# Optimization experiments

Measured on AMD Instinct MI355X. Metric: run time of the kernel, lower is better.

The kernel has to match this reference:

```python
import jax, jax.numpy as jnp
import numpy as np

D_MODEL = 1024
D_STATE = 16
D_CONV = 4
EXPAND = 2
D_INNER = EXPAND * D_MODEL        # 2048
DT_RANK = D_MODEL // 16           # ceil(1024/16) = 64
B, L = 2, 2048


def setup_inputs() -> dict:
    key = jax.random.key(0)
    ks = jax.random.split(key, 8)
    def init(k, shape, fan_in):
        return jax.random.normal(k, shape, jnp.float32) / np.sqrt(fan_in).astype(np.float32)
    x = jax.random.normal(ks[0], (B, L, D_MODEL), jnp.float32)
    W_in = init(ks[1], (2 * D_INNER, D_MODEL), D_MODEL)
    conv_w = init(ks[2], (D_INNER, 1, D_CONV), D_CONV)      # depthwise kernel (O, I/groups, K)
    conv_b = jnp.zeros((D_INNER,), jnp.float32)
    W_x = init(ks[3], (DT_RANK + 2 * D_STATE, D_INNER), D_INNER)
    W_dt = init(ks[4], (D_INNER, DT_RANK), DT_RANK)
    b_dt = jnp.zeros((D_INNER,), jnp.float32)
    A_log = jnp.log(jnp.tile(jnp.arange(1, D_STATE + 1, dtype=jnp.float32), (D_INNER, 1)))
    D_param = jnp.ones((D_INNER,), jnp.float32)
    W_out = init(ks[5], (D_MODEL, D_INNER), D_INNER)
    return {"x": x, "W_in": W_in, "conv_w": conv_w, "conv_b": conv_b,
            "W_x": W_x, "W_dt": W_dt, "b_dt": b_dt, "A_log": A_log,
            "D_param": D_param, "W_out": W_out}


def _mamba_forward(x, W_in, conv_w, conv_b, W_x, W_dt, b_dt, A_log, D_param, W_out):
    b, l, d = x.shape
    # in_proj -> split into ssm path and gate residual
    x_and_res = x @ W_in.T                               # [b, l, 2*d_inner]
    x_m, res = jnp.split(x_and_res, 2, axis=-1)
    # causal depthwise conv1d (torch pads both sides d_conv-1 then slices [:l] == left-pad causal conv)
    xc = jnp.transpose(x_m, (0, 2, 1))                   # [b, d_inner, l]
    xc = jax.lax.conv_general_dilated(
        xc, conv_w, window_strides=(1,), padding=[(D_CONV - 1, 0)],
        dimension_numbers=('NCH', 'OIH', 'NCH'), feature_group_count=D_INNER)
    xc = xc + conv_b[None, :, None]
    x_m = jax.nn.silu(jnp.transpose(xc, (0, 2, 1)))      # [b, l, d_inner]
    # ssm parameterization
    A = -jnp.exp(A_log)                                  # [d_inner, n]
    x_dbl = x_m @ W_x.T                                  # [b, l, dt_rank + 2n]
    dlt, Bm, Cm = jnp.split(x_dbl, [DT_RANK, DT_RANK + D_STATE], axis=-1)
    delta = jax.nn.softplus(dlt @ W_dt.T + b_dt)         # [b, l, d_inner]
    # selective scan over time
    def step(h, inp):
        d_i, B_i, C_i, x_i = inp                         # [b,d_in], [b,n], [b,n], [b,d_in]
        dA = jnp.exp(d_i[..., None] * A)                 # [b, d_in, n]
        h = dA * h + (d_i * x_i)[..., None] * B_i[:, None, :]
        y = jnp.einsum('bdn,bn->bd', h, C_i)
        return h, y
    h0 = jnp.zeros((b, D_INNER, D_STATE), x.dtype)
    seq = (jnp.transpose(delta, (1, 0, 2)), jnp.transpose(Bm, (1, 0, 2)),
           jnp.transpose(Cm, (1, 0, 2)), jnp.transpose(x_m, (1, 0, 2)))
    _, ys = jax.lax.scan(step, h0, seq)                  # [l, b, d_inner]
    y = jnp.transpose(ys, (1, 0, 2)) + D_param * x_m     # [b, l, d_inner]
    y = y * jax.nn.silu(res)
    return y @ W_out.T                                   # [b, l, d_model]


def reference(x, W_in, conv_w, conv_b, W_x, W_dt, b_dt, A_log, D_param, W_out):
    return _mamba_forward(x, W_in, conv_w, conv_b, W_x, W_dt, b_dt, A_log, D_param, W_out)
```

## Files before the change

kernel.cpp:

```cpp
#include <hip/hip_runtime.h>

typedef unsigned short u16;
typedef __attribute__((ext_vector_type(8))) short bf16x8;
typedef __attribute__((ext_vector_type(4))) float f32x4;

#define B_SZ   2
#define L_SZ   2048
#define DM     1024
#define DI     2048
#define NST    16
#define RNK    64
#define TOK    (B_SZ * L_SZ)
#define NC     128
#define CLEN   (L_SZ / NC)
#define XDS    128
#define KSPL   8

__device__ __forceinline__ float bf2f(u16 u) {
    return __uint_as_float(((unsigned int)u) << 16);
}
__device__ __forceinline__ u16 f2bf(float f) {
    unsigned int x = __float_as_uint(f);
    x += 0x7fffu + ((x >> 16) & 1u);
    return (u16)(x >> 16);
}
__device__ __forceinline__ float silu(float v) {
    return v / (1.f + __expf(-v));
}
__device__ __forceinline__ float softplus_f(float v) {
    return (v > 20.f) ? v : log1pf(__expf(v));
}
__device__ __forceinline__ void gload16(const u16* g, u16* l) {
    __builtin_amdgcn_global_load_lds(
        (const __attribute__((address_space(1))) void*)g,
        (__attribute__((address_space(3))) void*)l, 16, 0, 0);
}
__device__ __forceinline__ ushort4 cvt4(const float4 v) {
    ushort4 o;
    o.x = f2bf(v.x); o.y = f2bf(v.y); o.z = f2bf(v.z); o.w = f2bf(v.w);
    return o;
}

#define Q_XB   1048576
#define Q_WIN  (Q_XB + 1048576)
#define Q_WOUT (Q_WIN + 524288)
#define Q_WX   (Q_WOUT + 65536)
#define Q_WDT  (Q_WX + 32768)
__global__ __launch_bounds__(256)
void cvt_all(const float4* __restrict__ x,  const float4* __restrict__ Wi,
             const float4* __restrict__ Wo, const float4* __restrict__ Wx,
             const float4* __restrict__ Wd,
             ushort4* __restrict__ xb,  ushort4* __restrict__ Wib,
             ushort4* __restrict__ Wob, ushort4* __restrict__ Wxb,
             ushort4* __restrict__ Wdb)
{
    const int i = blockIdx.x * 256 + threadIdx.x;
    if (i < Q_XB) {
        xb[i] = cvt4(x[i]);
    } else if (i < Q_WIN) {
        const int j = i - Q_XB;  Wib[j] = cvt4(Wi[j]);
    } else if (i < Q_WOUT) {
        const int j = i - Q_WIN; Wob[j] = cvt4(Wo[j]);
    } else if (i < Q_WX) {
        const int j = i - Q_WOUT;
        const int row = (j * 4) >> 11;
        if (row < 96) Wxb[j] = cvt4(Wx[j]);
        else          Wxb[j] = (ushort4){0, 0, 0, 0};
    } else if (i < Q_WDT) {
        const int j = i - Q_WX;  Wdb[j] = cvt4(Wd[j]);
    }
}

template<int EPI>
__global__ __launch_bounds__(256, 2)
void gemm_bt(const u16* __restrict__ A, const u16* __restrict__ B,
             const int K, const int N,
             u16* __restrict__ out0, u16* __restrict__ out1,
             float* __restrict__ outF, const float* __restrict__ bias)
{
    __shared__ u16 sA[128 * 32];
    __shared__ u16 sB[128 * 32];

    const int tid  = threadIdx.x;
    const int rowBase = blockIdx.x << 7;
    const int colBase = blockIdx.y << 7;
    const int wave = tid >> 6, lane = tid & 63;
    const int wm = (wave >> 1) << 6;
    const int wn = (wave & 1) << 6;
    const int lrow = lane & 15, quad = lane >> 4;

    const int sr  = tid >> 2;
    const int skc = tid & 3;
    const u16* Ap = A + (size_t)(rowBase + sr) * K + skc * 8;
    const u16* Bp = B + (size_t)(colBase + sr) * K + skc * 8;
    const size_t rowJump = (size_t)64 * K;
    u16* lA0 = &sA[tid * 8];
    u16* lA1 = &sA[64 * 32 + tid * 8];
    u16* lB0 = &sB[tid * 8];
    u16* lB1 = &sB[64 * 32 + tid * 8];

    f32x4 acc[4][4];
#pragma unroll
    for (int i = 0; i < 4; ++i)
#pragma unroll
        for (int j = 0; j < 4; ++j) acc[i][j] = (f32x4){0.f, 0.f, 0.f, 0.f};

    const int KT = K >> 5;
    for (int kt = 0; kt < KT; ++kt) {
        const int ko = kt * 32;
        gload16(Ap + ko, lA0);
        gload16(Ap + ko + rowJump, lA1);
        gload16(Bp + ko, lB0);
        gload16(Bp + ko + rowJump, lB1);
        __syncthreads();

        bf16x8 af[4], bfr[4];
#pragma unroll
        for (int i = 0; i < 4; ++i)
            af[i] = *(const bf16x8*)&sA[(wm + i * 16 + lrow) * 32 + quad * 8];
#pragma unroll
        for (int j = 0; j < 4; ++j)
            bfr[j] = *(const bf16x8*)&sB[(wn + j * 16 + lrow) * 32 + quad * 8];

#pragma unroll
        for (int i = 0; i < 4; ++i)
#pragma unroll
            for (int j = 0; j < 4; ++j)
                acc[i][j] = __builtin_amdgcn_mfma_f32_16x16x32_bf16(
                    bfr[j], af[i], acc[i][j], 0, 0, 0);
        __syncthreads();
    }

#pragma unroll
    for (int i = 0; i < 4; ++i) {
        const int token = rowBase + wm + i * 16 + lrow;
#pragma unroll
        for (int j = 0; j < 4; ++j) {
            const int ch = colBase + wn + j * 16 + quad * 4;
            const f32x4 v = acc[i][j];
            if (EPI == 0) {
                *(float4*)&outF[(size_t)token * N + ch] =
                    (float4){v[0], v[1], v[2], v[3]};
            } else if (EPI == 2) {
                const float4 bb = *(const float4*)&bias[ch];
                ushort4 o;
                o.x = f2bf(softplus_f(v[0] + bb.x));
                o.y = f2bf(softplus_f(v[1] + bb.y));
                o.z = f2bf(softplus_f(v[2] + bb.z));
                o.w = f2bf(softplus_f(v[3] + bb.w));
                *(ushort4*)&out0[(size_t)token * N + ch] = o;
            } else {
                if (ch < DI) {
                    ushort4 o;
                    o.x = f2bf(v[0]); o.y = f2bf(v[1]);
                    o.z = f2bf(v[2]); o.w = f2bf(v[3]);
                    *(ushort4*)&out0[(size_t)token * DI + ch] = o;
                } else {
                    ushort4 o;
                    o.x = f2bf(silu(v[0])); o.y = f2bf(silu(v[1]));
                    o.z = f2bf(silu(v[2])); o.w = f2bf(silu(v[3]));
                    *(ushort4*)&out1[(size_t)token * DI + (ch - DI)] = o;
                }
            }
        }
    }
}

__global__ __launch_bounds__(256, 2)
void gemm_xdbl(const u16* __restrict__ A, const u16* __restrict__ B,
               float* __restrict__ part)
{
    __shared__ u16 sA[128 * 32];
    __shared__ u16 sB[128 * 32];

    const int tid  = threadIdx.x;
    const int rowBase = blockIdx.x << 7;
    const int ks   = blockIdx.y;
    const int k0   = ks * (DI / KSPL);
    const int wave = tid >> 6, lane = tid & 63;
    const int wm = (wave >> 1) << 6;
    const int wn = (wave & 1) << 6;
    const int lrow = lane & 15, quad = lane >> 4;

    const int sr  = tid >> 2;
    const int skc = tid & 3;
    const u16* Ap = A + (size_t)(rowBase + sr) * DI + k0 + skc * 8;
    const u16* Bp = B + (size_t)sr * DI + k0 + skc * 8;
    const size_t rowJump = (size_t)64 * DI;
    u16* lA0 = &sA[tid * 8];
    u16* lA1 = &sA[64 * 32 + tid * 8];
    u16* lB0 = &sB[tid * 8];
    u16* lB1 = &sB[64 * 32 + tid * 8];

    f32x4 acc[4][4];
#pragma unroll
    for (int i = 0; i < 4; ++i)
#pragma unroll
        for (int j = 0; j < 4; ++j) acc[i][j] = (f32x4){0.f, 0.f, 0.f, 0.f};

    const int KT = (DI / KSPL) >> 5;
    for (int kt = 0; kt < KT; ++kt) {
        const int ko = kt * 32;
        gload16(Ap + ko, lA0);
        gload16(Ap + ko + rowJump, lA1);
        gload16(Bp + ko, lB0);
        gload16(Bp + ko + rowJump, lB1);
        __syncthreads();

        bf16x8 af[4], bfr[4];
#pragma unroll
        for (int i = 0; i < 4; ++i)
            af[i] = *(const bf16x8*)&sA[(wm + i * 16 + lrow) * 32 + quad * 8];
#pragma unroll
        for (int j = 0; j < 4; ++j)
            bfr[j] = *(const bf16x8*)&sB[(wn + j * 16 + lrow) * 32 + quad * 8];

#pragma unroll
        for (int i = 0; i < 4; ++i)
#pragma unroll
            for (int j = 0; j < 4; ++j)
                acc[i][j] = __builtin_amdgcn_mfma_f32_16x16x32_bf16(
                    bfr[j], af[i], acc[i][j], 0, 0, 0);
        __syncthreads();
    }

    float* base = part + (size_t)ks * TOK * XDS;
#pragma unroll
    for (int i = 0; i < 4; ++i) {
        const int token = rowBase + wm + i * 16 + lrow;
#pragma unroll
        for (int j = 0; j < 4; ++j) {
            const int ch = wn + j * 16 + quad * 4;
            const f32x4 v = acc[i][j];
            *(float4*)&base[(size_t)token * XDS + ch] =
                (float4){v[0], v[1], v[2], v[3]};
        }
    }
}

__global__ __launch_bounds__(256)
void reduce_part(const float4* __restrict__ part, float4* __restrict__ xdbl,
                 u16* __restrict__ dltB)
{
    const int i = blockIdx.x * 256 + threadIdx.x;
    const int n4 = TOK * XDS / 4;
    float4 s = part[i];
#pragma unroll
    for (int ks = 1; ks < KSPL; ++ks) {
        const float4 v = part[(size_t)ks * n4 + i];
        s.x += v.x; s.y += v.y; s.z += v.z; s.w += v.w;
    }
    xdbl[i] = s;
    const int col4 = (i & (XDS / 4 - 1)) * 4;
    if (col4 < RNK) {
        const int row = i >> 5;
        *(ushort4*)(dltB + (size_t)row * RNK + col4) = cvt4(s);
    }
}

__global__ __launch_bounds__(256)
void conv_silu_kernel(const u16* __restrict__ xm, const float* __restrict__ cw,
                      const float* __restrict__ cb, u16* __restrict__ xc)
{
    const int idx = blockIdx.x * 256 + threadIdx.x;
    const int ch = idx & (DI - 1);
    const int t  = idx >> 11;
    const int l  = t & (L_SZ - 1);

    const float4 wv = *(const float4*)(cw + ch * 4);

    float acc = cb[ch];
    if (l >= 3) acc += wv.x * bf2f(xm[(size_t)(t - 3) * DI + ch]);
    if (l >= 2) acc += wv.y * bf2f(xm[(size_t)(t - 2) * DI + ch]);
    if (l >= 1) acc += wv.z * bf2f(xm[(size_t)(t - 1) * DI + ch]);
    acc += wv.w * bf2f(xm[(size_t)t * DI + ch]);

    xc[idx] = f2bf(silu(acc));
}

__global__ __launch_bounds__(256)
void scan_pass1(const u16* __restrict__ delta, const float* __restrict__ xdbl,
                const u16* __restrict__ xc, const float* __restrict__ A_log,
                float* __restrict__ hfin, float* __restrict__ Ssum)
{
    const int tid = threadIdx.x;
    const int ch  = blockIdx.x * 256 + tid;
    const int b   = blockIdx.y / NC;
    const int c   = blockIdx.y % NC;
    const int t0  = b * L_SZ + c * CLEN;

    __shared__ float sB[CLEN][16];
    {
        const int i = tid >> 4, nn = tid & 15;
        sB[i][nn] = xdbl[(size_t)(t0 + i) * XDS + 64 + nn];
    }

    float A[16];
    {
        const float4* Ar = (const float4*)(A_log + (size_t)ch * 16);
#pragma unroll
        for (int k = 0; k < 4; ++k) {
            const float4 v = Ar[k];
            A[4*k+0] = -__expf(v.x); A[4*k+1] = -__expf(v.y);
            A[4*k+2] = -__expf(v.z); A[4*k+3] = -__expf(v.w);
        }
    }
    __syncthreads();

    float h[16];
#pragma unroll
    for (int n = 0; n < 16; ++n) h[n] = 0.f;
    float S = 0.f;

    float d  = bf2f(delta[(size_t)t0 * DI + ch]);
    float xv = bf2f(xc[(size_t)t0 * DI + ch]);

    for (int i = 0; i < CLEN; ++i) {
        const int in_ = (i + 1 < CLEN) ? (i + 1) : i;
        const float dn = bf2f(delta[(size_t)(t0 + in_) * DI + ch]);
        const float xn = bf2f(xc[(size_t)(t0 + in_) * DI + ch]);
        const float dx = d * xv;
        S += d;
#pragma unroll
        for (int k = 0; k < 4; ++k) {
            const float4 Bv = *(const float4*)&sB[i][k * 4];
#pragma unroll
            for (int j = 0; j < 4; ++j) {
                const int n = k * 4 + j;
                const float e = __expf(d * A[n]);
                h[n] = e * h[n] + dx * (&Bv.x)[j];
            }
        }
        d = dn; xv = xn;
    }

    float* hp = hfin + ((size_t)(b * NC + c) * DI + ch) * 16;
#pragma unroll
    for (int k = 0; k < 4; ++k)
        *(float4*)(hp + 4 * k) = (float4){h[4*k], h[4*k+1], h[4*k+2], h[4*k+3]};
    Ssum[(size_t)(b * NC + c) * DI + ch] = S;
}

__global__ __launch_bounds__(256)
void scan_combine(const float* __restrict__ hfin, const float* __restrict__ Ssum,
                  const float* __restrict__ A_log, u16* __restrict__ h0buf)
{
    const int idx  = blockIdx.x * 256 + threadIdx.x;
    const int b    = idx >> 15;
    const int base = idx & 32767;
    const int ch   = base >> 4;
    const float A  = -__expf(A_log[base]);
    float h0 = 0.f;
#pragma unroll 4
    for (int c = 0; c < NC; ++c) {
        const size_t o = (size_t)(b * NC + c) * 32768 + base;
        h0buf[o] = f2bf(h0);
        const float S = Ssum[(size_t)(b * NC + c) * DI + ch];
        h0 = hfin[o] + __expf(A * S) * h0;
    }
}

__global__ __launch_bounds__(256)
void scan_pass2(const u16* __restrict__ delta, const float* __restrict__ xdbl,
                const u16* __restrict__ xc, const u16* __restrict__ sres,
                const float* __restrict__ A_log, const float* __restrict__ Dp,
                const u16* __restrict__ h0buf, u16* __restrict__ yfin)
{
    const int tid = threadIdx.x;
    const int ch  = blockIdx.x * 256 + tid;
    const int b   = blockIdx.y / NC;
    const int c   = blockIdx.y % NC;
    const int t0  = b * L_SZ + c * CLEN;

    __shared__ float sB[CLEN][16], sC[CLEN][16];
    {
        const int i = tid >> 4, nn = tid & 15;
        sB[i][nn] = xdbl[(size_t)(t0 + i) * XDS + 64 + nn];
        sC[i][nn] = xdbl[(size_t)(t0 + i) * XDS + 80 + nn];
    }

    float A[16];
    {
        const float4* Ar = (const float4*)(A_log + (size_t)ch * 16);
#pragma unroll
        for (int k = 0; k < 4; ++k) {
            const float4 v = Ar[k];
            A[4*k+0] = -__expf(v.x); A[4*k+1] = -__expf(v.y);
            A[4*k+2] = -__expf(v.z); A[4*k+3] = -__expf(v.w);
        }
    }
    const float Dval = Dp[ch];

    float h[16];
    {
        const u16* hp = h0buf + (size_t)(b * NC + c) * 32768 + (size_t)ch * 16;
#pragma unroll
        for (int k = 0; k < 4; ++k) {
            const ushort4 q = *(const ushort4*)(hp + 4 * k);
            h[4*k+0] = bf2f(q.x); h[4*k+1] = bf2f(q.y);
            h[4*k+2] = bf2f(q.z); h[4*k+3] = bf2f(q.w);
        }
    }
    __syncthreads();

    float d  = bf2f(delta[(size_t)t0 * DI + ch]);
    float xv = bf2f(xc[(size_t)t0 * DI + ch]);
    float rv = bf2f(sres[(size_t)t0 * DI + ch]);

    for (int i = 0; i < CLEN; ++i) {
        const int in_ = (i + 1 < CLEN) ? (i + 1) : i;
        const float dn = bf2f(delta[(size_t)(t0 + in_) * DI + ch]);
        const float xn = bf2f(xc[(size_t)(t0 + in_) * DI + ch]);
        const float rn = bf2f(sres[(size_t)(t0 + in_) * DI + ch]);
        const float dx = d * xv;
        float acc0 = 0.f, acc1 = 0.f, acc2 = 0.f, acc3 = 0.f;
#pragma unroll
        for (int k = 0; k < 4; ++k) {
            const float4 Bv = *(const float4*)&sB[i][k * 4];
            const float4 Cv = *(const float4*)&sC[i][k * 4];
#pragma unroll
            for (int j = 0; j < 4; ++j) {
                const int n = k * 4 + j;
                const float e = __expf(d * A[n]);
                h[n] = e * h[n] + dx * (&Bv.x)[j];
                const float t = h[n] * (&Cv.x)[j];
                if (j == 0) acc0 += t; else if (j == 1) acc1 += t;
                else if (j == 2) acc2 += t; else acc3 += t;
            }
        }
        const float p = (acc0 + acc1) + (acc2 + acc3);
        const float y = (p + Dval * xv) * rv;
        yfin[(size_t)(t0 + i) * DI + ch] = f2bf(y);
        d = dn; xv = xn; rv = rn;
    }
}

extern "C" void kernel_launch(void* const* d_in, const int* in_sizes, int n_in,
                              void* d_out, int out_size, void* d_ws, size_t ws_size,
                              hipStream_t stream)
{
    const float* x      = (const float*)d_in[0];
    const float* W_in   = (const float*)d_in[1];
    const float* conv_w = (const float*)d_in[2];
    const float* conv_b = (const float*)d_in[3];
    const float* W_x    = (const float*)d_in[4];
    const float* W_dt   = (const float*)d_in[5];
    const float* b_dt   = (const float*)d_in[6];
    const float* A_log  = (const float*)d_in[7];
    const float* D_par  = (const float*)d_in[8];
    const float* W_out  = (const float*)d_in[9];
    float* out = (float*)d_out;

    char* ws = (char*)d_ws;
    size_t off = 0;
    u16* xb    = (u16*)(ws + off); off += (size_t)TOK * DM * 2;
    u16* Winb  = (u16*)(ws + off); off += (size_t)(2 * DI) * DM * 2;
    u16* Woutb = (u16*)(ws + off); off += (size_t)DM * DI * 2;
    u16* Wxb   = (u16*)(ws + off); off += (size_t)XDS * DI * 2;
    u16* Wdtb  = (u16*)(ws + off); off += (size_t)DI * RNK * 2;
    u16* dltB  = (u16*)(ws + off); off += (size_t)TOK * RNK * 2;
    u16* xm    = (u16*)(ws + off); off += (size_t)TOK * DI * 2;
    u16* xc    = (u16*)(ws + off); off += (size_t)TOK * DI * 2;
    u16* sres  = (u16*)(ws + off); off += (size_t)TOK * DI * 2;
    float* xdblP = (float*)(ws + off); off += (size_t)TOK * XDS * 4;
    u16* dlt16   = (u16*)(ws + off);   off += (size_t)TOK * DI * 2;
    float* hfin  = (float*)(ws + off); off += (size_t)NC * B_SZ * DI * NST * 4;
    u16* h0buf   = (u16*)(ws + off);   off += (size_t)NC * B_SZ * DI * NST * 2;
    float* Ssum  = (float*)(ws + off); off += (size_t)NC * B_SZ * DI * 4;
    u16* yfin = xm;
    float* part = hfin;

    cvt_all<<<(Q_WDT + 255) / 256, 256, 0, stream>>>(
        (const float4*)x, (const float4*)W_in, (const float4*)W_out,
        (const float4*)W_x, (const float4*)W_dt,
        (ushort4*)xb, (ushort4*)Winb, (ushort4*)Woutb,
        (ushort4*)Wxb, (ushort4*)Wdtb);

    gemm_bt<1><<<dim3(TOK / 128, (2 * DI) / 128), 256, 0, stream>>>(
        xb, Winb, DM, 2 * DI, xm, sres, nullptr, nullptr);

    conv_silu_kernel<<<(TOK * DI) / 256, 256, 0, stream>>>(xm, conv_w, conv_b, xc);

    gemm_xdbl<<<dim3(TOK / 128, KSPL), 256, 0, stream>>>(xc, Wxb, part);
    reduce_part<<<(TOK * XDS / 4) / 256, 256, 0, stream>>>(
        (const float4*)part, (float4*)xdblP, dltB);

    gemm_bt<2><<<dim3(TOK / 128, DI / 128), 256, 0, stream>>>(
        dltB, Wdtb, RNK, DI, dlt16, nullptr, nullptr, b_dt);

    scan_pass1<<<dim3(DI / 256, B_SZ * NC), 256, 0, stream>>>(
        dlt16, xdblP, xc, A_log, hfin, Ssum);
    scan_combine<<<(B_SZ * DI * NST) / 256, 256, 0, stream>>>(
        hfin, Ssum, A_log, h0buf);
    scan_pass2<<<dim3(DI / 256, B_SZ * NC), 256, 0, stream>>>(
        dlt16, xdblP, xc, sres, A_log, D_par, h0buf, yfin);

    gemm_bt<0><<<dim3(TOK / 128, DM / 128), 256, 0, stream>>>(
        yfin, Woutb, DI, DM, nullptr, nullptr, out, nullptr);
}
```

Before: 342.4 us.

## Fuse delta projection and softplus into scan passes; store chunk states as bf16

Drops the standalone dt-projection GEMM and the full-size bf16 delta buffer. Each scan block now computes its own 16x256 delta tile with MFMA from the low-rank dt input and W_dt, applies bias and softplus, and keeps the tile in shared memory. Both scan passes redo this small GEMM, trading a little duplicated compute for no delta write/read traffic and one fewer launch. Per-chunk final states are also stored as bf16 instead of fp32, which halves that traffic but lowers the precision of the inter-chunk carry.

```diff
diff --git a/kernel.cpp b/kernel.cpp
--- a/kernel.cpp
+++ b/kernel.cpp
@@ -15,6 +15,7 @@
 #define CLEN   (L_SZ / NC)
 #define XDS    128
 #define KSPL   8
+#define SDP    260
 
 __device__ __forceinline__ float bf2f(u16 u) {
     return __uint_as_float(((unsigned int)u) << 16);
@@ -39,6 +40,31 @@
     ushort4 o;
     o.x = f2bf(v.x); o.y = f2bf(v.y); o.z = f2bf(v.z); o.w = f2bf(v.w);
     return o;
+}
+
+__device__ __forceinline__ void delta_tile(
+    const u16* __restrict__ dltB, const u16* __restrict__ Wdtb,
+    const float* __restrict__ bdt, int t0, int ch0, int tid,
+    u16 (*sD)[SDP])
+{
+    const int wave = tid >> 6, lane = tid & 63;
+    const int lrow = lane & 15, quad = lane >> 4;
+    const bf16x8 af0 = *(const bf16x8*)&dltB[(size_t)(t0 + lrow) * RNK + quad * 8];
+    const bf16x8 af1 = *(const bf16x8*)&dltB[(size_t)(t0 + lrow) * RNK + 32 + quad * 8];
+#pragma unroll
+    for (int jj = 0; jj < 4; ++jj) {
+        const int cb = (wave * 4 + jj) * 16;
+        const bf16x8 b0 = *(const bf16x8*)&Wdtb[(size_t)(ch0 + cb + lrow) * RNK + quad * 8];
+        const bf16x8 b1 = *(const bf16x8*)&Wdtb[(size_t)(ch0 + cb + lrow) * RNK + 32 + quad * 8];
+        f32x4 acc = (f32x4){0.f, 0.f, 0.f, 0.f};
+        acc = __builtin_amdgcn_mfma_f32_16x16x32_bf16(b0, af0, acc, 0, 0, 0);
+        acc = __builtin_amdgcn_mfma_f32_16x16x32_bf16(b1, af1, acc, 0, 0, 0);
+#pragma unroll
+        for (int r = 0; r < 4; ++r) {
+            const int cl = cb + quad * 4 + r;
+            sD[lrow][cl] = f2bf(softplus_f(acc[r] + bdt[ch0 + cl]));
+        }
+    }
 }
 
 #define Q_XB   1048576
@@ -76,7 +102,7 @@
 void gemm_bt(const u16* __restrict__ A, const u16* __restrict__ B,
              const int K, const int N,
              u16* __restrict__ out0, u16* __restrict__ out1,
-             float* __restrict__ outF, const float* __restrict__ bias)
+             float* __restrict__ outF)
 {
     __shared__ u16 sA[128 * 32];
     __shared__ u16 sB[128 * 32];
@@ -141,14 +167,6 @@
             if (EPI == 0) {
                 *(float4*)&outF[(size_t)token * N + ch] =
                     (float4){v[0], v[1], v[2], v[3]};
-            } else if (EPI == 2) {
-                const float4 bb = *(const float4*)&bias[ch];
-                ushort4 o;
-                o.x = f2bf(softplus_f(v[0] + bb.x));
-                o.y = f2bf(softplus_f(v[1] + bb.y));
-                o.z = f2bf(softplus_f(v[2] + bb.z));
-                o.w = f2bf(softplus_f(v[3] + bb.w));
-                *(ushort4*)&out0[(size_t)token * N + ch] = o;
             } else {
                 if (ch < DI) {
                     ushort4 o;
@@ -279,17 +297,22 @@
 }
 
 __global__ __launch_bounds__(256)
-void scan_pass1(const u16* __restrict__ delta, const float* __restrict__ xdbl,
+void scan_pass1(const u16* __restrict__ dltB, const float* __restrict__ xdbl,
                 const u16* __restrict__ xc, const float* __restrict__ A_log,
-                float* __restrict__ hfin, float* __restrict__ Ssum)
+                const float* __restrict__ bdt, const u16* __restrict__ Wdtb,
+                u16* __restrict__ hfin, float* __restrict__ Ssum)
 {
     const int tid = threadIdx.x;
-    const int ch  = blockIdx.x * 256 + tid;
+    const int ch0 = blockIdx.x * 256;
+    const int ch  = ch0 + tid;
     const int b   = blockIdx.y / NC;
     const int c   = blockIdx.y % NC;
     const int t0  = b * L_SZ + c * CLEN;
 
     __shared__ float sB[CLEN][16];
+    __shared__ u16 sD[CLEN][SDP];
+
+    delta_tile(dltB, Wdtb, bdt, t0, ch0, tid, sD);
     {
         const int i = tid >> 4, nn = tid & 15;
         sB[i][nn] = xdbl[(size_t)(t0 + i) * XDS + 64 + nn];
@@ -312,13 +335,12 @@
     for (int n = 0; n < 16; ++n) h[n] = 0.f;
     float S = 0.f;
 
-    float d  = bf2f(delta[(size_t)t0 * DI + ch]);
     float xv = bf2f(xc[(size_t)t0 * DI + ch]);
 
     for (int i = 0; i < CLEN; ++i) {
         const int in_ = (i + 1 < CLEN) ? (i + 1) : i;
-        const float dn = bf2f(delta[(size_t)(t0 + in_) * DI + ch]);
         const float xn = bf2f(xc[(size_t)(t0 + in_) * DI + ch]);
+        const float d  = bf2f(sD[i][tid]);
         const float dx = d * xv;
         S += d;
 #pragma unroll
@@ -331,18 +353,22 @@
                 h[n] = e * h[n] + dx * (&Bv.x)[j];
             }
         }
-        d = dn; xv = xn;
-    }
-
-    float* hp = hfin + ((size_t)(b * NC + c) * DI + ch) * 16;
-#pragma unroll
-    for (int k = 0; k < 4; ++k)
-        *(float4*)(hp + 4 * k) = (float4){h[4*k], h[4*k+1], h[4*k+2], h[4*k+3]};
+        xv = xn;
+    }
+
+    u16* hp = hfin + ((size_t)(b * NC + c) * DI + ch) * 16;
+#pragma unroll
+    for (int k = 0; k < 4; ++k) {
+        ushort4 o;
+        o.x = f2bf(h[4*k]); o.y = f2bf(h[4*k+1]);
+        o.z = f2bf(h[4*k+2]); o.w = f2bf(h[4*k+3]);
+        *(ushort4*)(hp + 4 * k) = o;
+    }
     Ssum[(size_t)(b * NC + c) * DI + ch] = S;
 }
 
 __global__ __launch_bounds__(256)
-void scan_combine(const float* __restrict__ hfin, const float* __restrict__ Ssum,
+void scan_combine(const u16* __restrict__ hfin, const float* __restrict__ Ssum,
                   const float* __restrict__ A_log, u16* __restrict__ h0buf)
 {
     const int idx  = blockIdx.x * 256 + threadIdx.x;
@@ -356,23 +382,28 @@
         const size_t o = (size_t)(b * NC + c) * 32768 + base;
         h0buf[o] = f2bf(h0);
         const float S = Ssum[(size_t)(b * NC + c) * DI + ch];
-        h0 = hfin[o] + __expf(A * S) * h0;
+        h0 = bf2f(hfin[o]) + __expf(A * S) * h0;
     }
 }
 
 __global__ __launch_bounds__(256)
-void scan_pass2(const u16* __restrict__ delta, const float* __restrict__ xdbl,
+void scan_pass2(const u16* __restrict__ dltB, const float* __restrict__ xdbl,
                 const u16* __restrict__ xc, const u16* __restrict__ sres,
                 const float* __restrict__ A_log, const float* __restrict__ Dp,
+                const float* __restrict__ bdt, const u16* __restrict__ Wdtb,
                 const u16* __restrict__ h0buf, u16* __restrict__ yfin)
 {
     const int tid = threadIdx.x;
-    const int ch  = blockIdx.x * 256 + tid;
+    const int ch0 = blockIdx.x * 256;
+    const int ch  = ch0 + tid;
     const int b   = blockIdx.y / NC;
     const int c   = blockIdx.y % NC;
     const int t0  = b * L_SZ + c * CLEN;
 
     __shared__ float sB[CLEN][16], sC[CLEN][16];
+    __shared__ u16 sD[CLEN][SDP];
+
+    delta_tile(dltB, Wdtb, bdt, t0, ch0, tid, sD);
     {
         const int i = tid >> 4, nn = tid & 15;
         sB[i][nn] = xdbl[(size_t)(t0 + i) * XDS + 64 + nn];
@@ -403,15 +434,14 @@
     }
     __syncthreads();
 
-    float d  = bf2f(delta[(size_t)t0 * DI + ch]);
     float xv = bf2f(xc[(size_t)t0 * DI + ch]);
     float rv = bf2f(sres[(size_t)t0 * DI + ch]);
 
     for (int i = 0; i < CLEN; ++i) {
         const int in_ = (i + 1 < CLEN) ? (i + 1) : i;
-        const float dn = bf2f(delta[(size_t)(t0 + in_) * DI + ch]);
         const float xn = bf2f(xc[(size_t)(t0 + in_) * DI + ch]);
         const float rn = bf2f(sres[(size_t)(t0 + in_) * DI + ch]);
+        const float d  = bf2f(sD[i][tid]);
         const float dx = d * xv;
         float acc0 = 0.f, acc1 = 0.f, acc2 = 0.f, acc3 = 0.f;
 #pragma unroll
@@ -431,7 +461,7 @@
         const float p = (acc0 + acc1) + (acc2 + acc3);
         const float y = (p + Dval * xv) * rv;
         yfin[(size_t)(t0 + i) * DI + ch] = f2bf(y);
-        d = dn; xv = xn; rv = rn;
+        xv = xn; rv = rn;
     }
 }
 
@@ -463,12 +493,11 @@
     u16* xc    = (u16*)(ws + off); off += (size_t)TOK * DI * 2;
     u16* sres  = (u16*)(ws + off); off += (size_t)TOK * DI * 2;
     float* xdblP = (float*)(ws + off); off += (size_t)TOK * XDS * 4;
-    u16* dlt16   = (u16*)(ws + off);   off += (size_t)TOK * DI * 2;
-    float* hfin  = (float*)(ws + off); off += (size_t)NC * B_SZ * DI * NST * 4;
+    u16* hfin    = (u16*)(ws + off);   off += (size_t)NC * B_SZ * DI * NST * 2;
     u16* h0buf   = (u16*)(ws + off);   off += (size_t)NC * B_SZ * DI * NST * 2;
     float* Ssum  = (float*)(ws + off); off += (size_t)NC * B_SZ * DI * 4;
     u16* yfin = xm;
-    float* part = hfin;
+    float* part = (float*)hfin;
 
     cvt_all<<<(Q_WDT + 255) / 256, 256, 0, stream>>>(
         (const float4*)x, (const float4*)W_in, (const float4*)W_out,
@@ -477,7 +506,7 @@
         (ushort4*)Wxb, (ushort4*)Wdtb);
 
     gemm_bt<1><<<dim3(TOK / 128, (2 * DI) / 128), 256, 0, stream>>>(
-        xb, Winb, DM, 2 * DI, xm, sres, nullptr, nullptr);
+        xb, Winb, DM, 2 * DI, xm, sres, nullptr);
 
     conv_silu_kernel<<<(TOK * DI) / 256, 256, 0, stream>>>(xm, conv_w, conv_b, xc);
 
@@ -485,16 +514,13 @@
     reduce_part<<<(TOK * XDS / 4) / 256, 256, 0, stream>>>(
         (const float4*)part, (float4*)xdblP, dltB);
 
-    gemm_bt<2><<<dim3(TOK / 128, DI / 128), 256, 0, stream>>>(
-        dltB, Wdtb, RNK, DI, dlt16, nullptr, nullptr, b_dt);
-
     scan_pass1<<<dim3(DI / 256, B_SZ * NC), 256, 0, stream>>>(
-        dlt16, xdblP, xc, A_log, hfin, Ssum);
+        dltB, xdblP, xc, A_log, b_dt, Wdtb, hfin, Ssum);
     scan_combine<<<(B_SZ * DI * NST) / 256, 256, 0, stream>>>(
         hfin, Ssum, A_log, h0buf);
     scan_pass2<<<dim3(DI / 256, B_SZ * NC), 256, 0, stream>>>(
-        dlt16, xdblP, xc, sres, A_log, D_par, h0buf, yfin);
+        dltB, xdblP, xc, sres, A_log, D_par, b_dt, Wdtb, h0buf, yfin);
 
     gemm_bt<0><<<dim3(TOK / 128, DM / 128), 256, 0, stream>>>(
-        yfin, Woutb, DI, DM, nullptr, nullptr, out, nullptr);
-}
+        yfin, Woutb, DI, DM, nullptr, nullptr, out);
+}
```

Measured after the change: 350.5 us. +2.4%, slower.
